# Kernel tuning notes

Hardware: AMD Instinct MI355X
Metric: run time of the kernel (lower is better)

## Reference

```python
import jax, jax.numpy as jnp
import numpy as np

N, C, E = 50000, 128, 10
INV3 = float(1.0 / np.sqrt(3.0))
NORM_C = float(1.0 / np.sqrt(C))


def setup_inputs() -> dict:
    key = jax.random.key(0)
    ks = jax.random.split(key, 14)
    node_feats = jax.random.normal(ks[0], (N, 4 * C), jnp.float32)
    elem = jax.random.randint(ks[1], (N,), 0, E)
    node_attrs = jax.nn.one_hot(elem, E, dtype=jnp.float32)
    sc = jax.random.normal(ks[2], (N, 4 * C), jnp.float32)
    tp2_w = jax.random.normal(ks[3], (4, C), jnp.float32)
    tp3_w = jax.random.normal(ks[4], (8, C), jnp.float32)
    coef0_w0 = jax.random.normal(ks[5], (E, C, C), jnp.float32)
    coef0_w1 = jax.random.normal(ks[6], (E, C, C), jnp.float32)
    coef1_w0 = jax.random.normal(ks[7], (E, 2 * C, C), jnp.float32)
    coef1_w1 = jax.random.normal(ks[8], (E, 2 * C, C), jnp.float32)
    coef2_w0 = jax.random.normal(ks[9], (E, 4 * C, C), jnp.float32)
    coef2_w1 = jax.random.normal(ks[10], (E, 4 * C, C), jnp.float32)
    lin_w0 = jax.random.normal(ks[11], (C, C), jnp.float32)
    lin_w1 = jax.random.normal(ks[12], (C, C), jnp.float32)
    return dict(node_feats=node_feats, node_attrs=node_attrs, sc=sc,
                tp2_w=tp2_w, tp3_w=tp3_w,
                coef0_w0=coef0_w0, coef0_w1=coef0_w1,
                coef1_w0=coef1_w0, coef1_w1=coef1_w1,
                coef2_w0=coef2_w0, coef2_w1=coef2_w1,
                lin_w0=lin_w0, lin_w1=lin_w1)


def acc_elem_linear(x0, x1, attrs, W0, W1):
    # per-element linear combine: one-hot attrs select element-specific weights
    norm = 1.0 / np.sqrt(x0.shape[1])
    o0 = jnp.zeros((attrs.shape[0], W0.shape[2]), x0.dtype)
    o1 = jnp.zeros((attrs.shape[0], W1.shape[2], 3), x1.dtype)
    for e in range(W0.shape[0]):  # small fixed element count
        a = attrs[:, e]
        o0 = o0 + a[:, None] * (x0 @ W0[e])
        o1 = o1 + a[:, None, None] * jnp.einsum('ncm,cd->ndm', x1, W1[e])
    return o0 * norm, o1 * norm


def reference(node_feats, node_attrs, sc, tp2_w, tp3_w,
              coef0_w0, coef0_w1, coef1_w0, coef1_w1,
              coef2_w0, coef2_w1, lin_w0, lin_w1):
    n = node_feats.shape[0]
    s = node_feats[:, :C]                      # [N,C]    0e
    v = node_feats[:, C:].reshape(n, C, 3)     # [N,C,3]  1o

    # nu=2: channelwise (uuu) CG tensor product, paths filtered to {0e,1o}
    m0a = tp2_w[0] * s * s                                # 0e x 0e -> 0e
    m1a = tp2_w[1][:, None] * s[:, :, None] * v * INV3    # 0e x 1o -> 1o
    m1b = tp2_w[2][:, None] * v * s[:, :, None] * INV3    # 1o x 0e -> 1o
    m0b = tp2_w[3] * jnp.sum(v * v, axis=-1) * INV3       # 1o x 1o -> 0e

    # nu=3: mid (A0=m0a 0e, A1=m1a 1o, A2=m1b 1o, A3=m0b 0e) x node_feats
    q0 = jnp.concatenate([
        tp3_w[0] * m0a * s,
        tp3_w[3] * jnp.sum(m1a * v, -1) * INV3,
        tp3_w[5] * jnp.sum(m1b * v, -1) * INV3,
        tp3_w[6] * m0b * s], axis=1)                      # [N,4C]
    q1 = jnp.concatenate([
        tp3_w[1][:, None] * m0a[:, :, None] * v * INV3,
        tp3_w[2][:, None] * m1a * s[:, :, None] * INV3,
        tp3_w[4][:, None] * m1b * s[:, :, None] * INV3,
        tp3_w[7][:, None] * m0b[:, :, None] * v * INV3], axis=1)  # [N,4C,3]

    f0, f1 = acc_elem_linear(s, v, node_attrs, coef0_w0, coef0_w1)
    g0, g1 = acc_elem_linear(jnp.concatenate([m0a, m0b], 1),
                             jnp.concatenate([m1a, m1b], 1),
                             node_attrs, coef1_w0, coef1_w1)
    h0, h1 = acc_elem_linear(q0, q1, node_attrs, coef2_w0, coef2_w1)
    o0 = f0 + g0 + h0
    o1 = f1 + g1 + h1

    o0 = (o0 @ lin_w0) * NORM_C
    o1 = jnp.einsum('ncm,cd->ndm', o1, lin_w1) * NORM_C
    out = jnp.concatenate([o0, o1.reshape(n, -1)], axis=1) + sc
    return out
```

## Files before the change

### kernel.cpp

```cpp
#include <hip/hip_runtime.h>

typedef unsigned short u16;
typedef __attribute__((ext_vector_type(8))) short short8;
typedef __attribute__((ext_vector_type(4))) float f32x4;

#define N_NODES 50000
#define C_ 128
#define E_ 10
#define NT_ 16
#define NBLK_MAIN 3200
#define K0_ 640
#define K1_ 512

#define WF0_BYTES (E_ * 8 * 20 * 512 * 2)
#define WF1_BYTES (E_ * 8 * 16 * 512 * 2)
#define CNT_OFF   (WF0_BYTES + WF1_BYTES)
#define LIST_OFF  (CNT_OFF + 64)

__device__ __forceinline__ u16 f2bf(float f){ union{unsigned u; float f;} v; v.f = f; unsigned u = v.u; u += 0x7FFFu + ((u>>16)&1u); return (u16)(u>>16); }

__global__ void zero_cnt_kernel(int* __restrict__ cnt) {
    if (threadIdx.x < E_) cnt[threadIdx.x] = 0;
}

__global__ __launch_bounds__(256) void prep_weights_kernel(
    const float* __restrict__ tp2, const float* __restrict__ tp3,
    const float* __restrict__ c00, const float* __restrict__ c10, const float* __restrict__ c20,
    const float* __restrict__ c01, const float* __restrict__ c11, const float* __restrict__ c21,
    const float* __restrict__ lin0, const float* __restrict__ lin1,
    u16* __restrict__ WF0, u16* __restrict__ WF1)
{
    const int b = blockIdx.x;
    const int e = b / 9, kb = b % 9;
    const int which = (kb >= 5) ? 1 : 0;
    const int seg = which ? kb - 5 : kb;
    const float* __restrict__ lin = which ? lin1 : lin0;

    __shared__ u16 R[128 * 136];
    __shared__ u16 LT[128 * 132];

    const int tid = threadIdx.x;
    const float NC = 0.08838834764831845f;

    for (int t = tid; t < 128 * 32; t += 256) {
        const int jj = t >> 5, c4 = (t & 31) << 2;
        const float4 v = *(const float4*)(lin + jj * 128 + c4);
        LT[(c4 + 0) * 132 + jj] = f2bf(v.x * NC);
        LT[(c4 + 1) * 132 + jj] = f2bf(v.y * NC);
        LT[(c4 + 2) * 132 + jj] = f2bf(v.z * NC);
        LT[(c4 + 3) * 132 + jj] = f2bf(v.w * NC);
    }

    {
        const int c = tid >> 1, jh = (tid & 1) * 64;
        const float i128 = 0.08838834764831845f;
        const float i256 = 0.0625f;
        const float i512 = 0.04419417382415922f;
        const float I3   = 0.5773502691896258f;
        const float I9   = I3 * I3;
        const float t2_0 = tp2[0*C_+c], t2_1 = tp2[1*C_+c], t2_2 = tp2[2*C_+c], t2_3 = tp2[3*C_+c];
        const float t3_0 = tp3[0*C_+c], t3_1 = tp3[1*C_+c], t3_2 = tp3[2*C_+c];
        const float t3_3 = tp3[3*C_+c], t3_4 = tp3[4*C_+c], t3_5 = tp3[5*C_+c];
        const float t3_6 = tp3[6*C_+c], t3_7 = tp3[7*C_+c];

        const float* P0; const float* P1 = nullptr; const float* P2 = nullptr;
        float a0 = 0.f, a1 = 0.f, a2 = 0.f;
        if (!which) {
            const float* C0 = c00 + (size_t)e * C_   * C_;
            const float* C1 = c10 + (size_t)e * 2*C_ * C_;
            const float* C2 = c20 + (size_t)e * 4*C_ * C_;
            switch (seg) {
            case 0: P0 = C0 + c*C_;          a0 = i128; break;
            case 1: P0 = C1 + c*C_;          a0 = t2_0 * i256; break;
            case 2: P0 = C1 + (C_+c)*C_;     a0 = t2_3 * I3 * i256; break;
            case 3: P0 = C2 + c*C_;          a0 = t3_0 * t2_0 * i512; break;
            default:
// ... 56 lines not shown
#pragma unroll
        for (int s = 0; s < 2; ++s) {
            const int krow = (wv + s * 4) * 16 + lcol;
            union { unsigned long long q[2]; short8 v; } ua;
            ua.q[0] = *(const unsigned long long*)&R[krow * 136 + jj0];
            ua.q[1] = *(const unsigned long long*)&R[krow * 136 + jj0 + 16];
#pragma unroll
            for (int t = 0; t < 8; ++t)
                acc[s][t] = __builtin_amdgcn_mfma_f32_16x16x32_bf16(ua.v, bf[t], acc[s][t], 0, 0, 0);
        }
    }

#pragma unroll
    for (int s = 0; s < 2; ++s) {
#pragma unroll
        for (int r = 0; r < 4; ++r) {
            const int k = (wv + s * 4) * 16 + 4 * gD + r;
            const int ks = k >> 5, r2 = k & 31;
            const int eh = r2 >> 4, g2 = (r2 >> 2) & 3, el = r2 & 3;
            const int elem = eh * 4 + el;
            const int lanef = lcol + 16 * g2;
            const int slot = seg * 4 + ks;
#pragma unroll
            for (int t = 0; t < 8; ++t) {
                const u16 wvl = f2bf(acc[s][t][r]);
                if (!which) WF0[(((size_t)(e*8 + t))*20 + slot)*512 + lanef*8 + elem] = wvl;
                else        WF1[(((size_t)(e*8 + t))*16 + slot)*512 + lanef*8 + elem] = wvl;
            }
        }
    }
}

__global__ void bucket_kernel(const float* __restrict__ attrs,
                              int* __restrict__ cnt, int* __restrict__ lists)
{
    __shared__ int lcnt[E_];
    __shared__ int lbase[E_];
    const int n = blockIdx.x * 256 + threadIdx.x;
    if (threadIdx.x < E_) lcnt[threadIdx.x] = 0;
    __syncthreads();
    int e = 0, my = 0;
    if (n < N_NODES) {
        const float* a = attrs + (size_t)n * E_;
#pragma unroll
        for (int i = 0; i < E_; ++i) if (a[i] > 0.5f) e = i;
        my = atomicAdd(&lcnt[e], 1);
    }
    __syncthreads();
    if (threadIdx.x < E_) lbase[threadIdx.x] = atomicAdd(&cnt[threadIdx.x], lcnt[threadIdx.x]);
    __syncthreads();
    if (n < N_NODES) lists[e*N_NODES + lbase[e] + my] = n;
}

__global__ __launch_bounds__(512, 4) void main_kernel(
    const float* __restrict__ feats, const float* __restrict__ sc,
    const int* __restrict__ cnt, const int* __restrict__ lists,
    const u16* __restrict__ WF0, const u16* __restrict__ WF1,
    float* __restrict__ out)
{
    __shared__ __align__(16) u16 Afull[68 * 512];

    const int tid = threadIdx.x;
    const int bx = blockIdx.x;

    int e = -1, tile = 0, accT = 0;
#pragma unroll
    for (int i = 0; i < E_; ++i) {
        const int ci = cnt[i];
        const int t = (ci + NT_ - 1) >> 4;
        if (e < 0 && bx < accT + t) { e = i; tile = bx - accT; }
        accT += t;
    }
    if (e < 0) return;
    const int nvalid = min(NT_, cnt[e] - tile * NT_);

    const int node = tid >> 5;
    const int ch   = tid & 31;
    const int n = (node < nvalid) ? lists[e*N_NODES + tile*NT_ + node] : -1;

    {
        const int cg = ch;
        float4 sv  = make_float4(0.f,0.f,0.f,0.f);
        float4 va  = sv, vb = sv, vc = sv;
        if (n >= 0) {
            const float* f = feats + (size_t)n * 512;
            sv = *(const float4*)(f + cg*4);
            va = *(const float4*)(f + 128 + cg*12);
            vb = *(const float4*)(f + 128 + cg*12 + 4);
            vc = *(const float4*)(f + 128 + cg*12 + 8);
        }
        float Sa[4]  = {sv.x, sv.y, sv.z, sv.w};
        float Va[12] = {va.x,va.y,va.z,va.w, vb.x,vb.y,vb.z,vb.w, vc.x,vc.y,vc.z,vc.w};

        u16 fsS[5][4];
        u16 fsV[4][3][4];
#pragma unroll
        for (int i = 0; i < 4; ++i) {
            const float S  = Sa[i];
            const float V0 = Va[3*i], V1 = Va[3*i+1], V2 = Va[3*i+2];
            const float S2 = S * S;
            const float VV = V0*V0 + V1*V1 + V2*V2;
            fsS[0][i] = f2bf(S);
            fsS[1][i] = f2bf(S2);
            fsS[2][i] = f2bf(VV);
            fsS[3][i] = f2bf(S2 * S);
            fsS[4][i] = f2bf(S * VV);
            const float Vm[3] = {V0, V1, V2};
#pragma unroll
            for (int m = 0; m < 3; ++m) {
                fsV[0][m][i] = f2bf(Vm[m]);
                fsV[1][m][i] = f2bf(S  * Vm[m]);
                fsV[2][m][i] = f2bf(S2 * Vm[m]);
                fsV[3][m][i] = f2bf(VV * Vm[m]);
            }
        }
        const int lane  = node + 16 * (cg & 3);
        const int ks    = cg >> 3;
        const int ebase = ((cg >> 2) & 1) * 4;
        const int lanep = lane ^ (ks << 1);
        u16* bp = &Afull[lanep*8 + ebase];
#pragma unroll
        for (int p = 0; p < 5; ++p)
            *(ushort4*)&bp[(p*4 + ks) * 512] = *(ushort4*)fsS[p];
#pragma unroll
        for (int q = 0; q < 4; ++q)
#pragma unroll
            for (int m = 0; m < 3; ++m)
                *(ushort4*)&bp[(20 + q*12 + m*4 + ks) * 512] = *(ushort4*)fsV[q][m];
    }
    __syncthreads();

    const int w = tid >> 6, l = tid & 63;
    const int lcol = l & 15, g = l >> 4;
    const int col = w*16 + lcol;
    const u16* WB0 = WF0 + ((size_t)(e*8 + w)) * 20 * 512 + l*8;
    const u16* WB1 = WF1 + ((size_t)(e*8 + w)) * 16 * 512 + l*8;

    f32x4 accS = {0.f, 0.f, 0.f, 0.f};
    f32x4 accV[3];
#pragma unroll
    for (int m = 0; m < 3; ++m) accV[m] = accS;

    float4 scR0, scR1, scR2, scR3;

    short8 bS[2][5], bV[2][4];
#pragma unroll
    for (int p = 0; p < 5; ++p) bS[0][p] = *(const short8*)(WB0 + (p*4 + 0) * 512);
#pragma unroll
    for (int q = 0; q < 4; ++q) bV[0][q] = *(const short8*)(WB1 + (q*4 + 0) * 512);

#pragma unroll
    for (int ks = 0; ks < 4; ++ks) {
        const int cur = ks & 1, nxt = cur ^ 1;
        if (ks < 3) {
#pragma unroll
            for (int p = 0; p < 5; ++p) bS[nxt][p] = *(const short8*)(WB0 + (p*4 + ks + 1) * 512);
#pragma unroll
            for (int q = 0; q < 4; ++q) bV[nxt][q] = *(const short8*)(WB1 + (q*4 + ks + 1) * 512);
        }
        if (ks == 3 && n >= 0) {
            const float* sp = sc + (size_t)n * 512 + ch * 4;
            scR0 = *(const float4*)(sp);
            scR1 = *(const float4*)(sp + 128);
            scR2 = *(const float4*)(sp + 256);
            scR3 = *(const float4*)(sp + 384);
        }
        const int lp8 = (l ^ (ks << 1)) * 8;
#pragma unroll
        for (int p = 0; p < 5; ++p) {
            const short8 a = *(const short8*)&Afull[(p*4 + ks)*512 + lp8];
            accS = __builtin_amdgcn_mfma_f32_16x16x32_bf16(a, bS[cur][p], accS, 0, 0, 0);
        }
#pragma unroll
        for (int q = 0; q < 4; ++q)
#pragma unroll
            for (int m = 0; m < 3; ++m) {
                const short8 a = *(const short8*)&Afull[(20 + q*12 + m*4 + ks)*512 + lp8];
                accV[m] = __builtin_amdgcn_mfma_f32_16x16x32_bf16(a, bV[cur][q], accV[m], 0, 0, 0);
            }
    }

    __syncthreads();
    float* OutB = (float*)Afull;
#pragma unroll
    for (int r = 0; r < 4; ++r) {
        const int nd = 4*g + r;
        OutB[nd*516 + col] = accS[r];
#pragma unroll
        for (int m = 0; m < 3; ++m)
            OutB[nd*516 + 128 + 3*col + m] = accV[m][r];
    }
    __syncthreads();

    if (n >= 0) {
        const size_t gb = (size_t)n * 512 + ch * 4;
        const float4 v0 = *(const float4*)&OutB[node*516 + ch*4];
        const float4 v1 = *(const float4*)&OutB[node*516 + ch*4 + 128];
        const float4 v2 = *(const float4*)&OutB[node*516 + ch*4 + 256];
        const float4 v3 = *(const float4*)&OutB[node*516 + ch*4 + 384];
        float4 o0, o1, o2, o3;
        o0.x=v0.x+scR0.x; o0.y=v0.y+scR0.y; o0.z=v0.z+scR0.z; o0.w=v0.w+scR0.w;
        o1.x=v1.x+scR1.x; o1.y=v1.y+scR1.y; o1.z=v1.z+scR1.z; o1.w=v1.w+scR1.w;
        o2.x=v2.x+scR2.x; o2.y=v2.y+scR2.y; o2.z=v2.z+scR2.z; o2.w=v2.w+scR2.w;
        o3.x=v3.x+scR3.x; o3.y=v3.y+scR3.y; o3.z=v3.z+scR3.z; o3.w=v3.w+scR3.w;
        *(float4*)(out + gb)       = o0;
        *(float4*)(out + gb + 128) = o1;
        *(float4*)(out + gb + 256) = o2;
        *(float4*)(out + gb + 384) = o3;
    }
}

extern "C" void kernel_launch(void* const* d_in, const int* in_sizes, int n_in,
                              void* d_out, int out_size, void* d_ws, size_t ws_size,
                              hipStream_t stream) {
    const float* feats = (const float*)d_in[0];
    const float* attrs = (const float*)d_in[1];
    const float* sc    = (const float*)d_in[2];
    const float* tp2   = (const float*)d_in[3];
    const float* tp3   = (const float*)d_in[4];
    const float* c00   = (const float*)d_in[5];
    const float* c01   = (const float*)d_in[6];
    const float* c10   = (const float*)d_in[7];
    const float* c11   = (const float*)d_in[8];
    const float* c20   = (const float*)d_in[9];
    const float* c21   = (const float*)d_in[10];
    const float* lin0  = (const float*)d_in[11];
    const float* lin1  = (const float*)d_in[12];
    float* out = (float*)d_out;

    char* ws = (char*)d_ws;
    u16* WF0   = (u16*)(ws);
    u16* WF1   = (u16*)(ws + WF0_BYTES);
    int* cnt   = (int*)(ws + CNT_OFF);
    int* lists = (int*)(ws + LIST_OFF);

    hipLaunchKernelGGL(zero_cnt_kernel, dim3(1), dim3(64), 0, stream, cnt);
    hipLaunchKernelGGL(prep_weights_kernel, dim3(E_*9), dim3(256), 0, stream,
                       tp2, tp3, c00, c10, c20, c01, c11, c21, lin0, lin1, WF0, WF1);
    hipLaunchKernelGGL(bucket_kernel, dim3((N_NODES + 255)/256), dim3(256), 0, stream,
                       attrs, cnt, lists);
    hipLaunchKernelGGL(main_kernel, dim3(NBLK_MAIN), dim3(512), 0, stream,
                       feats, sc, cnt, lists, WF0, WF1, out);
}
```

Before: 118.2 us.

## Make main kernel persistent with prefetch of next tile's features

```diff
diff --git a/kernel.cpp b/kernel.cpp
--- a/kernel.cpp
+++ b/kernel.cpp
@@ -8,7 +8,7 @@
 #define C_ 128
 #define E_ 10
 #define NT_ 16
-#define NBLK_MAIN 3200
+#define GRID_MAIN 512
 #define K0_ 640
 #define K1_ 512
 
@@ -18,10 +18,6 @@
 #define LIST_OFF  (CNT_OFF + 64)
 
 __device__ __forceinline__ u16 f2bf(float f){ union{unsigned u; float f;} v; v.f = f; unsigned u = v.u; u += 0x7FFFu + ((u>>16)&1u); return (u16)(u>>16); }
-
-__global__ void zero_cnt_kernel(int* __restrict__ cnt) {
-    if (threadIdx.x < E_) cnt[threadIdx.x] = 0;
-}
 
 __global__ __launch_bounds__(256) void prep_weights_kernel(
     const float* __restrict__ tp2, const float* __restrict__ tp3,
@@ -195,150 +191,182 @@
     const int tid = threadIdx.x;
     const int bx = blockIdx.x;
 
-    int e = -1, tile = 0, accT = 0;
-#pragma unroll
-    for (int i = 0; i < E_; ++i) {
-        const int ci = cnt[i];
-        const int t = (ci + NT_ - 1) >> 4;
-        if (e < 0 && bx < accT + t) { e = i; tile = bx - accT; }
-        accT += t;
-    }
-    if (e < 0) return;
-    const int nvalid = min(NT_, cnt[e] - tile * NT_);
+    int cr0 = cnt[0], cr1 = cnt[1], cr2 = cnt[2], cr3 = cnt[3], cr4 = cnt[4];
+    int cr5 = cnt[5], cr6 = cnt[6], cr7 = cnt[7], cr8 = cnt[8], cr9 = cnt[9];
+#define TC(x) (((x) + NT_ - 1) >> 4)
+    const int t0 = 0;
+    const int t1 = t0 + TC(cr0); const int t2 = t1 + TC(cr1);
+    const int t3 = t2 + TC(cr2); const int t4 = t3 + TC(cr3);
+    const int t5 = t4 + TC(cr4); const int t6 = t5 + TC(cr5);
+    const int t7 = t6 + TC(cr6); const int t8 = t7 + TC(cr7);
+    const int t9 = t8 + TC(cr8); const int ntiles = t9 + TC(cr9);
+#undef TC
 
     const int node = tid >> 5;
     const int ch   = tid & 31;
-    const int n = (node < nvalid) ? lists[e*N_NODES + tile*NT_ + node] : -1;
-
-    {
-        const int cg = ch;
-        float4 sv  = make_float4(0.f,0.f,0.f,0.f);
-        float4 va  = sv, vb = sv, vc = sv;
-        if (n >= 0) {
-            const float* f = feats + (size_t)n * 512;
-            sv = *(const float4*)(f + cg*4);
-            va = *(const float4*)(f + 128 + cg*12);
-            vb = *(const float4*)(f + 128 + cg*12 + 4);
-            vc = *(const float4*)(f + 128 + cg*12 + 8);
-        }
-        float Sa[4]  = {sv.x, sv.y, sv.z, sv.w};
-        float Va[12] = {va.x,va.y,va.z,va.w, vb.x,vb.y,vb.z,vb.w, vc.x,vc.y,vc.z,vc.w};
-
-        u16 fsS[5][4];
-        u16 fsV[4][3][4];
-#pragma unroll
-        for (int i = 0; i < 4; ++i) {
-            const float S  = Sa[i];
-            const float V0 = Va[3*i], V1 = Va[3*i+1], V2 = Va[3*i+2];
-            const float S2 = S * S;
-            const float VV = V0*V0 + V1*V1 + V2*V2;
-            fsS[0][i] = f2bf(S);
-            fsS[1][i] = f2bf(S2);
-            fsS[2][i] = f2bf(VV);
-            fsS[3][i] = f2bf(S2 * S);
-            fsS[4][i] = f2bf(S * VV);
-            const float Vm[3] = {V0, V1, V2};
-#pragma unroll
-            for (int m = 0; m < 3; ++m) {
-                fsV[0][m][i] = f2bf(Vm[m]);
-                fsV[1][m][i] = f2bf(S  * Vm[m]);
-                fsV[2][m][i] = f2bf(S2 * Vm[m]);
-                fsV[3][m][i] = f2bf(VV * Vm[m]);
-            }
-        }
-        const int lane  = node + 16 * (cg & 3);
-        const int ks    = cg >> 3;
-        const int ebase = ((cg >> 2) & 1) * 4;
-        const int lanep = lane ^ (ks << 1);
-        u16* bp = &Afull[lanep*8 + ebase];
-#pragma unroll
-        for (int p = 0; p < 5; ++p)
-            *(ushort4*)&bp[(p*4 + ks) * 512] = *(ushort4*)fsS[p];
-#pragma unroll
-        for (int q = 0; q < 4; ++q)
-#pragma unroll
-            for (int m = 0; m < 3; ++m)
-                *(ushort4*)&bp[(20 + q*12 + m*4 + ks) * 512] = *(ushort4*)fsV[q][m];
-    }
-    __syncthreads();
-
     const int w = tid >> 6, l = tid & 63;
     const int lcol = l & 15, g = l >> 4;
     const int col = w*16 + lcol;
-    const u16* WB0 = WF0 + ((size_t)(e*8 + w)) * 20 * 512 + l*8;
-    const u16* WB1 = WF1 + ((size_t)(e*8 + w)) * 16 * 512 + l*8;
-
-    f32x4 accS = {0.f, 0.f, 0.f, 0.f};
-    f32x4 accV[3];
-#pragma unroll
-    for (int m = 0; m < 3; ++m) accV[m] = accS;
-
-    float4 scR0, scR1, scR2, scR3;
-
-    short8 bS[2][5], bV[2][4];
-#pragma unroll
-    for (int p = 0; p < 5; ++p) bS[0][p] = *(const short8*)(WB0 + (p*4 + 0) * 512);
-#pragma unroll
-    for (int q = 0; q < 4; ++q) bV[0][q] = *(const short8*)(WB1 + (q*4 + 0) * 512);
-
-#pragma unroll
-    for (int ks = 0; ks < 4; ++ks) {
-        const int cur = ks & 1, nxt = cur ^ 1;
-        if (ks < 3) {
-#pragma unroll
-            for (int p = 0; p < 5; ++p) bS[nxt][p] = *(const short8*)(WB0 + (p*4 + ks + 1) * 512);
-#pragma unroll
-            for (int q = 0; q < 4; ++q) bV[nxt][q] = *(const short8*)(WB1 + (q*4 + ks + 1) * 512);
-        }
-        if (ks == 3 && n >= 0) {
-            const float* sp = sc + (size_t)n * 512 + ch * 4;
-            scR0 = *(const float4*)(sp);
-            scR1 = *(const float4*)(sp + 128);
-            scR2 = *(const float4*)(sp + 256);
-            scR3 = *(const float4*)(sp + 384);
-        }
-        const int lp8 = (l ^ (ks << 1)) * 8;
-#pragma unroll
-        for (int p = 0; p < 5; ++p) {
-            const short8 a = *(const short8*)&Afull[(p*4 + ks)*512 + lp8];
-            accS = __builtin_amdgcn_mfma_f32_16x16x32_bf16(a, bS[cur][p], accS, 0, 0, 0);
-        }
-#pragma unroll
-        for (int q = 0; q < 4; ++q)
-#pragma unroll
-            for (int m = 0; m < 3; ++m) {
-                const short8 a = *(const short8*)&Afull[(20 + q*12 + m*4 + ks)*512 + lp8];
-                accV[m] = __builtin_amdgcn_mfma_f32_16x16x32_bf16(a, bV[cur][q], accV[m], 0, 0, 0);
-            }
-    }
-
-    __syncthreads();
-    float* OutB = (float*)Afull;
-#pragma unroll
-    for (int r = 0; r < 4; ++r) {
-        const int nd = 4*g + r;
-        OutB[nd*516 + col] = accS[r];
-#pragma unroll
-        for (int m = 0; m < 3; ++m)
-            OutB[nd*516 + 128 + 3*col + m] = accV[m][r];
-    }
-    __syncthreads();
-
+
+    if (bx >= ntiles) return;
+
+    auto map_tile = [&](int t, int& e_, int& nn_) {
+        int e = 9, base = t9, c = cr9;
+        if (t < t1) { e = 0; base = t0; c = cr0; }
+        else if (t < t2) { e = 1; base = t1; c = cr1; }
+        else if (t < t3) { e = 2; base = t2; c = cr2; }
+        else if (t < t4) { e = 3; base = t3; c = cr3; }
+        else if (t < t5) { e = 4; base = t4; c = cr4; }
+        else if (t < t6) { e = 5; base = t5; c = cr5; }
+        else if (t < t7) { e = 6; base = t6; c = cr6; }
+        else if (t < t8) { e = 7; base = t7; c = cr7; }
+        else if (t < t9) { e = 8; base = t8; c = cr8; }
+        const int tile = t - base;
+        const int nv = min(NT_, c - tile * NT_);
+        e_ = e;
+        nn_ = (node < nv) ? lists[e*N_NODES + tile*NT_ + node] : -1;
+    };
+
+    int e, n;
+    map_tile(bx, e, n);
+    float4 f0 = make_float4(0,0,0,0), f1 = f0, f2 = f0, f3 = f0;
     if (n >= 0) {
-        const size_t gb = (size_t)n * 512 + ch * 4;
-        const float4 v0 = *(const float4*)&OutB[node*516 + ch*4];
-        const float4 v1 = *(const float4*)&OutB[node*516 + ch*4 + 128];
-        const float4 v2 = *(const float4*)&OutB[node*516 + ch*4 + 256];
-        const float4 v3 = *(const float4*)&OutB[node*516 + ch*4 + 384];
-        float4 o0, o1, o2, o3;
-        o0.x=v0.x+scR0.x; o0.y=v0.y+scR0.y; o0.z=v0.z+scR0.z; o0.w=v0.w+scR0.w;
-        o1.x=v1.x+scR1.x; o1.y=v1.y+scR1.y; o1.z=v1.z+scR1.z; o1.w=v1.w+scR1.w;
-        o2.x=v2.x+scR2.x; o2.y=v2.y+scR2.y; o2.z=v2.z+scR2.z; o2.w=v2.w+scR2.w;
-        o3.x=v3.x+scR3.x; o3.y=v3.y+scR3.y; o3.z=v3.z+scR3.z; o3.w=v3.w+scR3.w;
-        *(float4*)(out + gb)       = o0;
-        *(float4*)(out + gb + 128) = o1;
-        *(float4*)(out + gb + 256) = o2;
-        *(float4*)(out + gb + 384) = o3;
+        const float* f = feats + (size_t)n * 512;
+        f0 = *(const float4*)(f + ch*4);
+        f1 = *(const float4*)(f + 128 + ch*12);
+        f2 = *(const float4*)(f + 128 + ch*12 + 4);
+        f3 = *(const float4*)(f + 128 + ch*12 + 8);
+    }
+
+    for (int t = bx; t < ntiles; t += GRID_MAIN) {
+        {
+            float Sa[4]  = {f0.x, f0.y, f0.z, f0.w};
+            float Va[12] = {f1.x,f1.y,f1.z,f1.w, f2.x,f2.y,f2.z,f2.w, f3.x,f3.y,f3.z,f3.w};
+
+            u16 fsS[5][4];
+            u16 fsV[4][3][4];
+#pragma unroll
+            for (int i = 0; i < 4; ++i) {
+                const float S  = Sa[i];
+                const float V0 = Va[3*i], V1 = Va[3*i+1], V2 = Va[3*i+2];
+                const float S2 = S * S;
+                const float VV = V0*V0 + V1*V1 + V2*V2;
+                fsS[0][i] = f2bf(S);
+                fsS[1][i] = f2bf(S2);
+                fsS[2][i] = f2bf(VV);
+                fsS[3][i] = f2bf(S2 * S);
+                fsS[4][i] = f2bf(S * VV);
+                const float Vm[3] = {V0, V1, V2};
+#pragma unroll
+                for (int m = 0; m < 3; ++m) {
+                    fsV[0][m][i] = f2bf(Vm[m]);
+                    fsV[1][m][i] = f2bf(S  * Vm[m]);
+                    fsV[2][m][i] = f2bf(S2 * Vm[m]);
+                    fsV[3][m][i] = f2bf(VV * Vm[m]);
+                }
+            }
+            const int lane  = node + 16 * (ch & 3);
+            const int ks    = ch >> 3;
+            const int ebase = ((ch >> 2) & 1) * 4;
+            const int lanep = lane ^ (ks << 1);
+            u16* bp = &Afull[lanep*8 + ebase];
+#pragma unroll
+            for (int p = 0; p < 5; ++p)
+                *(ushort4*)&bp[(p*4 + ks) * 512] = *(ushort4*)fsS[p];
+#pragma unroll
+            for (int q = 0; q < 4; ++q)
+#pragma unroll
+                for (int m = 0; m < 3; ++m)
+                    *(ushort4*)&bp[(20 + q*12 + m*4 + ks) * 512] = *(ushort4*)fsV[q][m];
+        }
+        __syncthreads();
+
+        const u16* WB0 = WF0 + ((size_t)(e*8 + w)) * (20*512) + l*8;
+        const u16* WB1 = WF1 + ((size_t)(e*8 + w)) * (16*512) + l*8;
+
+        f32x4 accS = {0.f, 0.f, 0.f, 0.f};
+        f32x4 accV0 = accS, accV1 = accS, accV2 = accS;
+        float4 scR0, scR1, scR2, scR3;
+        int ne = e, nn = -1;
+
+#pragma unroll
+        for (int ks = 0; ks < 4; ++ks) {
+            short8 bS[5], bV[4];
+#pragma unroll
+            for (int p = 0; p < 5; ++p) bS[p] = *(const short8*)(WB0 + (p*4 + ks) * 512);
+#pragma unroll
+            for (int q = 0; q < 4; ++q) bV[q] = *(const short8*)(WB1 + (q*4 + ks) * 512);
+
+            if (ks == 1 && n >= 0) {
+                const float* sp = sc + (size_t)n * 512 + ch * 4;
+                scR0 = *(const float4*)(sp);
+                scR1 = *(const float4*)(sp + 128);
+                scR2 = *(const float4*)(sp + 256);
+                scR3 = *(const float4*)(sp + 384);
+            }
+            if (ks == 2) {
+                const int tn = t + GRID_MAIN;
+                f0 = make_float4(0,0,0,0); f1 = f0; f2 = f0; f3 = f0;
+                if (tn < ntiles) {
+                    map_tile(tn, ne, nn);
+                    if (nn >= 0) {
+                        const float* f = feats + (size_t)nn * 512;
+                        f0 = *(const float4*)(f + ch*4);
+                        f1 = *(const float4*)(f + 128 + ch*12);
+                        f2 = *(const float4*)(f + 128 + ch*12 + 4);
+                        f3 = *(const float4*)(f + 128 + ch*12 + 8);
+                    }
+                }
+            }
+
+            const int lp8 = (l ^ (ks << 1)) * 8;
+#pragma unroll
+            for (int p = 0; p < 5; ++p) {
+                const short8 a = *(const short8*)&Afull[(p*4 + ks)*512 + lp8];
+                accS = __builtin_amdgcn_mfma_f32_16x16x32_bf16(a, bS[p], accS, 0, 0, 0);
+            }
+#pragma unroll
+            for (int q = 0; q < 4; ++q) {
+                const short8 a0 = *(const short8*)&Afull[(20 + q*12 + 0*4 + ks)*512 + lp8];
+                accV0 = __builtin_amdgcn_mfma_f32_16x16x32_bf16(a0, bV[q], accV0, 0, 0, 0);
+                const short8 a1 = *(const short8*)&Afull[(20 + q*12 + 1*4 + ks)*512 + lp8];
+                accV1 = __builtin_amdgcn_mfma_f32_16x16x32_bf16(a1, bV[q], accV1, 0, 0, 0);
+                const short8 a2 = *(const short8*)&Afull[(20 + q*12 + 2*4 + ks)*512 + lp8];
+                accV2 = __builtin_amdgcn_mfma_f32_16x16x32_bf16(a2, bV[q], accV2, 0, 0, 0);
+            }
+        }
+
+        __syncthreads();
+        float* OutB = (float*)Afull;
+#pragma unroll
+        for (int r = 0; r < 4; ++r) {
+            const int nd = 4*g + r;
+            OutB[nd*516 + col] = accS[r];
+            OutB[nd*516 + 128 + 3*col + 0] = accV0[r];
+            OutB[nd*516 + 128 + 3*col + 1] = accV1[r];
+            OutB[nd*516 + 128 + 3*col + 2] = accV2[r];
+        }
+        __syncthreads();
+
+        if (n >= 0) {
+            const size_t gb = (size_t)n * 512 + ch * 4;
+            const float4 v0 = *(const float4*)&OutB[node*516 + ch*4];
+            const float4 v1 = *(const float4*)&OutB[node*516 + ch*4 + 128];
+            const float4 v2 = *(const float4*)&OutB[node*516 + ch*4 + 256];
+            const float4 v3 = *(const float4*)&OutB[node*516 + ch*4 + 384];
+            float4 o0, o1, o2, o3;
+            o0.x=v0.x+scR0.x; o0.y=v0.y+scR0.y; o0.z=v0.z+scR0.z; o0.w=v0.w+scR0.w;
+            o1.x=v1.x+scR1.x; o1.y=v1.y+scR1.y; o1.z=v1.z+scR1.z; o1.w=v1.w+scR1.w;
+            o2.x=v2.x+scR2.x; o2.y=v2.y+scR2.y; o2.z=v2.z+scR2.z; o2.w=v2.w+scR2.w;
+            o3.x=v3.x+scR3.x; o3.y=v3.y+scR3.y; o3.z=v3.z+scR3.z; o3.w=v3.w+scR3.w;
+            *(float4*)(out + gb)       = o0;
+            *(float4*)(out + gb + 128) = o1;
+            *(float4*)(out + gb + 256) = o2;
+            *(float4*)(out + gb + 384) = o3;
+        }
+        __syncthreads();
+
+        e = ne; n = nn;
     }
 }
 
@@ -366,11 +394,11 @@
     int* cnt   = (int*)(ws + CNT_OFF);
     int* lists = (int*)(ws + LIST_OFF);
 
-    hipLaunchKernelGGL(zero_cnt_kernel, dim3(1), dim3(64), 0, stream, cnt);
+    hipMemsetAsync(cnt, 0, 64, stream);
     hipLaunchKernelGGL(prep_weights_kernel, dim3(E_*9), dim3(256), 0, stream,
                        tp2, tp3, c00, c10, c20, c01, c11, c21, lin0, lin1, WF0, WF1);
     hipLaunchKernelGGL(bucket_kernel, dim3((N_NODES + 255)/256), dim3(256), 0, stream,
                        attrs, cnt, lists);
-    hipLaunchKernelGGL(main_kernel, dim3(NBLK_MAIN), dim3(512), 0, stream,
+    hipLaunchKernelGGL(main_kernel, dim3(GRID_MAIN), dim3(512), 0, stream,
                        feats, sc, cnt, lists, WF0, WF1, out);
 }
```

New measurement: 149.2 us. 26.3% more time.

## Stage A operands through double-buffered LDS phases to raise main kernel occupancy

Applied to the files above, without the earlier changes.

```diff
diff --git a/kernel.cpp b/kernel.cpp
--- a/kernel.cpp
+++ b/kernel.cpp
@@ -18,10 +18,6 @@
 #define LIST_OFF  (CNT_OFF + 64)
 
 __device__ __forceinline__ u16 f2bf(float f){ union{unsigned u; float f;} v; v.f = f; unsigned u = v.u; u += 0x7FFFu + ((u>>16)&1u); return (u16)(u>>16); }
-
-__global__ void zero_cnt_kernel(int* __restrict__ cnt) {
-    if (threadIdx.x < E_) cnt[threadIdx.x] = 0;
-}
 
 __global__ __launch_bounds__(256) void prep_weights_kernel(
     const float* __restrict__ tp2, const float* __restrict__ tp3,
@@ -184,13 +180,13 @@
     if (n < N_NODES) lists[e*N_NODES + lbase[e] + my] = n;
 }
 
-__global__ __launch_bounds__(512, 4) void main_kernel(
+__global__ __launch_bounds__(512, 6) void main_kernel(
     const float* __restrict__ feats, const float* __restrict__ sc,
     const int* __restrict__ cnt, const int* __restrict__ lists,
     const u16* __restrict__ WF0, const u16* __restrict__ WF1,
     float* __restrict__ out)
 {
-    __shared__ __align__(16) u16 Afull[68 * 512];
+    __shared__ __align__(16) u16 A2[2][24 * 512];
 
     const int tid = threadIdx.x;
     const int bx = blockIdx.x;
@@ -210,117 +206,166 @@
     const int ch   = tid & 31;
     const int n = (node < nvalid) ? lists[e*N_NODES + tile*NT_ + node] : -1;
 
+    float4 f0 = make_float4(0.f,0.f,0.f,0.f), f1 = f0, f2 = f0, f3 = f0;
+    if (n >= 0) {
+        const float* f = feats + (size_t)n * 512;
+        f0 = *(const float4*)(f + ch*4);
+        f1 = *(const float4*)(f + 128 + ch*12);
+        f2 = *(const float4*)(f + 128 + ch*12 + 4);
+        f3 = *(const float4*)(f + 128 + ch*12 + 8);
+    }
+    const float Sa[4]  = {f0.x, f0.y, f0.z, f0.w};
+    const float Va[12] = {f1.x,f1.y,f1.z,f1.w, f2.x,f2.y,f2.z,f2.w, f3.x,f3.y,f3.z,f3.w};
+
+    const int lane  = node + 16 * (ch & 3);
+    const int ksl   = ch >> 3;
+    const int ebase = ((ch >> 2) & 1) * 4;
+    const int lanep = lane ^ (ksl << 1);
+    u16* bpA = &A2[0][lanep*8 + ebase];
+    u16* bpB = &A2[1][lanep*8 + ebase];
+
     {
-        const int cg = ch;
-        float4 sv  = make_float4(0.f,0.f,0.f,0.f);
-        float4 va  = sv, vb = sv, vc = sv;
-        if (n >= 0) {
-            const float* f = feats + (size_t)n * 512;
-            sv = *(const float4*)(f + cg*4);
-            va = *(const float4*)(f + 128 + cg*12);
-            vb = *(const float4*)(f + 128 + cg*12 + 4);
-            vc = *(const float4*)(f + 128 + cg*12 + 8);
-        }
-        float Sa[4]  = {sv.x, sv.y, sv.z, sv.w};
-        float Va[12] = {va.x,va.y,va.z,va.w, vb.x,vb.y,vb.z,vb.w, vc.x,vc.y,vc.z,vc.w};
-
-        u16 fsS[5][4];
-        u16 fsV[4][3][4];
+        u16 fs[5][4];
 #pragma unroll
         for (int i = 0; i < 4; ++i) {
             const float S  = Sa[i];
             const float V0 = Va[3*i], V1 = Va[3*i+1], V2 = Va[3*i+2];
             const float S2 = S * S;
             const float VV = V0*V0 + V1*V1 + V2*V2;
-            fsS[0][i] = f2bf(S);
-            fsS[1][i] = f2bf(S2);
-            fsS[2][i] = f2bf(VV);
-            fsS[3][i] = f2bf(S2 * S);
-            fsS[4][i] = f2bf(S * VV);
-            const float Vm[3] = {V0, V1, V2};
-#pragma unroll
-            for (int m = 0; m < 3; ++m) {
-                fsV[0][m][i] = f2bf(Vm[m]);
-                fsV[1][m][i] = f2bf(S  * Vm[m]);
-                fsV[2][m][i] = f2bf(S2 * Vm[m]);
-                fsV[3][m][i] = f2bf(VV * Vm[m]);
-            }
-        }
-        const int lane  = node + 16 * (cg & 3);
-        const int ks    = cg >> 3;
-        const int ebase = ((cg >> 2) & 1) * 4;
-        const int lanep = lane ^ (ks << 1);
-        u16* bp = &Afull[lanep*8 + ebase];
+            fs[0][i] = f2bf(S);
+            fs[1][i] = f2bf(S2);
+            fs[2][i] = f2bf(VV);
+            fs[3][i] = f2bf(S2 * S);
+            fs[4][i] = f2bf(S * VV);
+        }
 #pragma unroll
         for (int p = 0; p < 5; ++p)
-            *(ushort4*)&bp[(p*4 + ks) * 512] = *(ushort4*)fsS[p];
-#pragma unroll
-        for (int q = 0; q < 4; ++q)
-#pragma unroll
-            for (int m = 0; m < 3; ++m)
-                *(ushort4*)&bp[(20 + q*12 + m*4 + ks) * 512] = *(ushort4*)fsV[q][m];
+            *(ushort4*)&bpA[(p*4 + ksl) * 512] = *(ushort4*)fs[p];
     }
     __syncthreads();
 
     const int w = tid >> 6, l = tid & 63;
     const int lcol = l & 15, g = l >> 4;
     const int col = w*16 + lcol;
-    const u16* WB0 = WF0 + ((size_t)(e*8 + w)) * 20 * 512 + l*8;
-    const u16* WB1 = WF1 + ((size_t)(e*8 + w)) * 16 * 512 + l*8;
+    const u16* WB0 = WF0 + ((size_t)(e*8 + w)) * (20*512) + l*8;
+    const u16* WB1 = WF1 + ((size_t)(e*8 + w)) * (16*512) + l*8;
 
     f32x4 accS = {0.f, 0.f, 0.f, 0.f};
-    f32x4 accV[3];
-#pragma unroll
-    for (int m = 0; m < 3; ++m) accV[m] = accS;
-
-    float4 scR0, scR1, scR2, scR3;
-
-    short8 bS[2][5], bV[2][4];
-#pragma unroll
-    for (int p = 0; p < 5; ++p) bS[0][p] = *(const short8*)(WB0 + (p*4 + 0) * 512);
-#pragma unroll
-    for (int q = 0; q < 4; ++q) bV[0][q] = *(const short8*)(WB1 + (q*4 + 0) * 512);
-
-#pragma unroll
-    for (int ks = 0; ks < 4; ++ks) {
-        const int cur = ks & 1, nxt = cur ^ 1;
-        if (ks < 3) {
-#pragma unroll
-            for (int p = 0; p < 5; ++p) bS[nxt][p] = *(const short8*)(WB0 + (p*4 + ks + 1) * 512);
-#pragma unroll
-            for (int q = 0; q < 4; ++q) bV[nxt][q] = *(const short8*)(WB1 + (q*4 + ks + 1) * 512);
-        }
-        if (ks == 3 && n >= 0) {
-            const float* sp = sc + (size_t)n * 512 + ch * 4;
-            scR0 = *(const float4*)(sp);
-            scR1 = *(const float4*)(sp + 128);
-            scR2 = *(const float4*)(sp + 256);
-            scR3 = *(const float4*)(sp + 384);
-        }
-        const int lp8 = (l ^ (ks << 1)) * 8;
+    f32x4 accV0 = accS, accV1 = accS, accV2 = accS;
+
+    {
+        u16 fs[6][4];
+#pragma unroll
+        for (int i = 0; i < 4; ++i) {
+            const float S  = Sa[i];
+            const float Vm[3] = {Va[3*i], Va[3*i+1], Va[3*i+2]};
+#pragma unroll
+            for (int m = 0; m < 3; ++m) {
+                fs[m][i]     = f2bf(Vm[m]);
+                fs[3+m][i]   = f2bf(S * Vm[m]);
+            }
+        }
+#pragma unroll
+        for (int t = 0; t < 6; ++t)
+            *(ushort4*)&bpB[(t*4 + ksl) * 512] = *(ushort4*)fs[t];
+    }
+#pragma unroll
+    for (int ks2 = 0; ks2 < 4; ++ks2) {
+        short8 bS[5];
+#pragma unroll
+        for (int p = 0; p < 5; ++p) bS[p] = *(const short8*)(WB0 + (p*4 + ks2) * 512);
+        const int lp8 = (l ^ (ks2 << 1)) * 8;
 #pragma unroll
         for (int p = 0; p < 5; ++p) {
-            const short8 a = *(const short8*)&Afull[(p*4 + ks)*512 + lp8];
-            accS = __builtin_amdgcn_mfma_f32_16x16x32_bf16(a, bS[cur][p], accS, 0, 0, 0);
-        }
-#pragma unroll
-        for (int q = 0; q < 4; ++q)
+            const short8 a = *(const short8*)&A2[0][(p*4 + ks2)*512 + lp8];
+            accS = __builtin_amdgcn_mfma_f32_16x16x32_bf16(a, bS[p], accS, 0, 0, 0);
+        }
+    }
+    __syncthreads();
+
+    {
+        u16 fs[6][4];
+#pragma unroll
+        for (int i = 0; i < 4; ++i) {
+            const float S  = Sa[i];
+            const float V0 = Va[3*i], V1 = Va[3*i+1], V2 = Va[3*i+2];
+            const float S2 = S * S;
+            const float VV = V0*V0 + V1*V1 + V2*V2;
+            const float Vm[3] = {V0, V1, V2};
 #pragma unroll
             for (int m = 0; m < 3; ++m) {
-                const short8 a = *(const short8*)&Afull[(20 + q*12 + m*4 + ks)*512 + lp8];
-                accV[m] = __builtin_amdgcn_mfma_f32_16x16x32_bf16(a, bV[cur][q], accV[m], 0, 0, 0);
-            }
-    }
-
-    __syncthreads();
-    float* OutB = (float*)Afull;
+                fs[m][i]   = f2bf(S2 * Vm[m]);
+                fs[3+m][i] = f2bf(VV * Vm[m]);
+            }
+        }
+#pragma unroll
+        for (int t = 0; t < 6; ++t)
+            *(ushort4*)&bpA[(t*4 + ksl) * 512] = *(ushort4*)fs[t];
+    }
+    float4 scR0 = make_float4(0.f,0.f,0.f,0.f), scR1 = scR0, scR2 = scR0, scR3 = scR0;
+    if (n >= 0) {
+        const float* sp = sc + (size_t)n * 512 + ch * 4;
+        scR0 = *(const float4*)(sp);
+        scR1 = *(const float4*)(sp + 128);
+        scR2 = *(const float4*)(sp + 256);
+        scR3 = *(const float4*)(sp + 384);
+    }
+#pragma unroll
+    for (int ks2 = 0; ks2 < 4; ++ks2) {
+        const short8 b0 = *(const short8*)(WB1 + (0*4 + ks2) * 512);
+        const short8 b1 = *(const short8*)(WB1 + (1*4 + ks2) * 512);
+        const int lp8 = (l ^ (ks2 << 1)) * 8;
+        {
+            const short8 a0 = *(const short8*)&A2[1][(0*4 + ks2)*512 + lp8];
+            accV0 = __builtin_amdgcn_mfma_f32_16x16x32_bf16(a0, b0, accV0, 0, 0, 0);
+            const short8 a1 = *(const short8*)&A2[1][(1*4 + ks2)*512 + lp8];
+            accV1 = __builtin_amdgcn_mfma_f32_16x16x32_bf16(a1, b0, accV1, 0, 0, 0);
+            const short8 a2 = *(const short8*)&A2[1][(2*4 + ks2)*512 + lp8];
+            accV2 = __builtin_amdgcn_mfma_f32_16x16x32_bf16(a2, b0, accV2, 0, 0, 0);
+        }
+        {
+            const short8 a0 = *(const short8*)&A2[1][(3*4 + ks2)*512 + lp8];
+            accV0 = __builtin_amdgcn_mfma_f32_16x16x32_bf16(a0, b1, accV0, 0, 0, 0);
+            const short8 a1 = *(const short8*)&A2[1][(4*4 + ks2)*512 + lp8];
+            accV1 = __builtin_amdgcn_mfma_f32_16x16x32_bf16(a1, b1, accV1, 0, 0, 0);
+            const short8 a2 = *(const short8*)&A2[1][(5*4 + ks2)*512 + lp8];
+            accV2 = __builtin_amdgcn_mfma_f32_16x16x32_bf16(a2, b1, accV2, 0, 0, 0);
+        }
+    }
+    __syncthreads();
+
+#pragma unroll
+    for (int ks2 = 0; ks2 < 4; ++ks2) {
+        const short8 b2 = *(const short8*)(WB1 + (2*4 + ks2) * 512);
+        const short8 b3 = *(const short8*)(WB1 + (3*4 + ks2) * 512);
+        const int lp8 = (l ^ (ks2 << 1)) * 8;
+        {
+            const short8 a0 = *(const short8*)&A2[0][(0*4 + ks2)*512 + lp8];
+            accV0 = __builtin_amdgcn_mfma_f32_16x16x32_bf16(a0, b2, accV0, 0, 0, 0);
+            const short8 a1 = *(const short8*)&A2[0][(1*4 + ks2)*512 + lp8];
+            accV1 = __builtin_amdgcn_mfma_f32_16x16x32_bf16(a1, b2, accV1, 0, 0, 0);
+            const short8 a2 = *(const short8*)&A2[0][(2*4 + ks2)*512 + lp8];
+            accV2 = __builtin_amdgcn_mfma_f32_16x16x32_bf16(a2, b2, accV2, 0, 0, 0);
+        }
+        {
+            const short8 a0 = *(const short8*)&A2[0][(3*4 + ks2)*512 + lp8];
+            accV0 = __builtin_amdgcn_mfma_f32_16x16x32_bf16(a0, b3, accV0, 0, 0, 0);
+            const short8 a1 = *(const short8*)&A2[0][(4*4 + ks2)*512 + lp8];
+            accV1 = __builtin_amdgcn_mfma_f32_16x16x32_bf16(a1, b3, accV1, 0, 0, 0);
+            const short8 a2 = *(const short8*)&A2[0][(5*4 + ks2)*512 + lp8];
+            accV2 = __builtin_amdgcn_mfma_f32_16x16x32_bf16(a2, b3, accV2, 0, 0, 0);
+        }
+    }
+    __syncthreads();
+
+    float* OutB = (float*)&A2[0][0];
 #pragma unroll
     for (int r = 0; r < 4; ++r) {
         const int nd = 4*g + r;
         OutB[nd*516 + col] = accS[r];
-#pragma unroll
-        for (int m = 0; m < 3; ++m)
-            OutB[nd*516 + 128 + 3*col + m] = accV[m][r];
+        OutB[nd*516 + 128 + 3*col + 0] = accV0[r];
+        OutB[nd*516 + 128 + 3*col + 1] = accV1[r];
+        OutB[nd*516 + 128 + 3*col + 2] = accV2[r];
     }
     __syncthreads();
 
@@ -366,7 +411,7 @@
     int* cnt   = (int*)(ws + CNT_OFF);
     int* lists = (int*)(ws + LIST_OFF);
 
-    hipLaunchKernelGGL(zero_cnt_kernel, dim3(1), dim3(64), 0, stream, cnt);
+    hipMemsetAsync(cnt, 0, 64, stream);
     hipLaunchKernelGGL(prep_weights_kernel, dim3(E_*9), dim3(256), 0, stream,
                        tp2, tp3, c00, c10, c20, c01, c11, c21, lin0, lin1, WF0, WF1);
     hipLaunchKernelGGL(bucket_kernel, dim3((N_NODES + 255)/256), dim3(256), 0, stream,
```

New measurement: 117.3 us. About the same (-0.7%).

## Restructure main kernel to 256 threads with staged double-buffered LDS A-tiles

Applied to the files above, without the earlier changes.

```diff
diff --git a/kernel.cpp b/kernel.cpp
--- a/kernel.cpp
+++ b/kernel.cpp
@@ -18,9 +18,10 @@
 #define LIST_OFF  (CNT_OFF + 64)
 
 __device__ __forceinline__ u16 f2bf(float f){ union{unsigned u; float f;} v; v.f = f; unsigned u = v.u; u += 0x7FFFu + ((u>>16)&1u); return (u16)(u>>16); }
-
-__global__ void zero_cnt_kernel(int* __restrict__ cnt) {
-    if (threadIdx.x < E_) cnt[threadIdx.x] = 0;
+__device__ __forceinline__ unsigned cvtpk(float a, float b){
+    unsigned r;
+    asm("v_cvt_pk_bf16_f32 %0, %1, %2" : "=v"(r) : "v"(a), "v"(b));
+    return r;
 }
 
 __global__ __launch_bounds__(256) void prep_weights_kernel(
@@ -184,13 +185,13 @@
     if (n < N_NODES) lists[e*N_NODES + lbase[e] + my] = n;
 }
 
-__global__ __launch_bounds__(512, 4) void main_kernel(
+__global__ __launch_bounds__(256, 3) void main_kernel(
     const float* __restrict__ feats, const float* __restrict__ sc,
     const int* __restrict__ cnt, const int* __restrict__ lists,
     const u16* __restrict__ WF0, const u16* __restrict__ WF1,
     float* __restrict__ out)
 {
-    __shared__ __align__(16) u16 Afull[68 * 512];
+    __shared__ __align__(16) u16 A2[2][24 * 512];
 
     const int tid = threadIdx.x;
     const int bx = blockIdx.x;
@@ -206,140 +207,167 @@
     if (e < 0) return;
     const int nvalid = min(NT_, cnt[e] - tile * NT_);
 
-    const int node = tid >> 5;
-    const int ch   = tid & 31;
+    const int node = tid >> 4;
+    const int cg   = tid & 15;
     const int n = (node < nvalid) ? lists[e*N_NODES + tile*NT_ + node] : -1;
 
-    {
-        const int cg = ch;
-        float4 sv  = make_float4(0.f,0.f,0.f,0.f);
-        float4 va  = sv, vb = sv, vc = sv;
-        if (n >= 0) {
-            const float* f = feats + (size_t)n * 512;
-            sv = *(const float4*)(f + cg*4);
-            va = *(const float4*)(f + 128 + cg*12);
-            vb = *(const float4*)(f + 128 + cg*12 + 4);
-            vc = *(const float4*)(f + 128 + cg*12 + 8);
-        }
-        float Sa[4]  = {sv.x, sv.y, sv.z, sv.w};
-        float Va[12] = {va.x,va.y,va.z,va.w, vb.x,vb.y,vb.z,vb.w, vc.x,vc.y,vc.z,vc.w};
-
-        u16 fsS[5][4];
-        u16 fsV[4][3][4];
-#pragma unroll
-        for (int i = 0; i < 4; ++i) {
-            const float S  = Sa[i];
-            const float V0 = Va[3*i], V1 = Va[3*i+1], V2 = Va[3*i+2];
-            const float S2 = S * S;
-            const float VV = V0*V0 + V1*V1 + V2*V2;
-            fsS[0][i] = f2bf(S);
-            fsS[1][i] = f2bf(S2);
-            fsS[2][i] = f2bf(VV);
-            fsS[3][i] = f2bf(S2 * S);
-            fsS[4][i] = f2bf(S * VV);
-            const float Vm[3] = {V0, V1, V2};
+    float4 s0 = make_float4(0.f,0.f,0.f,0.f), s1 = s0;
+    float4 v4[6];
+#pragma unroll
+    for (int k = 0; k < 6; ++k) v4[k] = s0;
+    if (n >= 0) {
+        const float* f = feats + (size_t)n * 512;
+        s0 = *(const float4*)(f + cg*8);
+        s1 = *(const float4*)(f + cg*8 + 4);
+#pragma unroll
+        for (int k = 0; k < 6; ++k) v4[k] = *(const float4*)(f + 128 + cg*24 + 4*k);
+    }
+    float S[8]  = {s0.x,s0.y,s0.z,s0.w, s1.x,s1.y,s1.z,s1.w};
+    float V[24] = {v4[0].x,v4[0].y,v4[0].z,v4[0].w, v4[1].x,v4[1].y,v4[1].z,v4[1].w,
+                   v4[2].x,v4[2].y,v4[2].z,v4[2].w, v4[3].x,v4[3].y,v4[3].z,v4[3].w,
+                   v4[4].x,v4[4].y,v4[4].z,v4[4].w, v4[5].x,v4[5].y,v4[5].z,v4[5].w};
+    float S2[8], VV[8];
+#pragma unroll
+    for (int i = 0; i < 8; ++i) {
+        S2[i] = S[i]*S[i];
+        VV[i] = V[3*i]*V[3*i] + V[3*i+1]*V[3*i+1] + V[3*i+2]*V[3*i+2];
+    }
+
+    const int ksl   = cg >> 2;
+    const int eh    = (cg >> 1) & 1;
+    const int gb    = (cg & 1) * 2;
+    const int lp0   = (node + 16*gb)        ^ (ksl << 1);
+    const int lp1   = (node + 16*(gb + 1))  ^ (ksl << 1);
+    const int off0  = lp0*8 + 4*eh;
+    const int off1  = lp1*8 + 4*eh;
+
+#define WSLOT(BUF, SLOT, V0,V1,V2,V3,V4,V5,V6,V7) do { \
+        uint2 w0_, w1_; \
+        w0_.x = cvtpk((V0),(V1)); w0_.y = cvtpk((V2),(V3)); \
+        w1_.x = cvtpk((V4),(V5)); w1_.y = cvtpk((V6),(V7)); \
+        *(uint2*)&A2[BUF][(SLOT)*512 + off0] = w0_; \
+        *(uint2*)&A2[BUF][(SLOT)*512 + off1] = w1_; \
+    } while (0)
+
+    WSLOT(0, 0*4 + ksl, S[0],S[1],S[2],S[3],S[4],S[5],S[6],S[7]);
+    WSLOT(0, 1*4 + ksl, S2[0],S2[1],S2[2],S2[3],S2[4],S2[5],S2[6],S2[7]);
+    WSLOT(0, 2*4 + ksl, VV[0],VV[1],VV[2],VV[3],VV[4],VV[5],VV[6],VV[7]);
+    WSLOT(0, 3*4 + ksl, S2[0]*S[0],S2[1]*S[1],S2[2]*S[2],S2[3]*S[3],
+                        S2[4]*S[4],S2[5]*S[5],S2[6]*S[6],S2[7]*S[7]);
+    WSLOT(0, 4*4 + ksl, S[0]*VV[0],S[1]*VV[1],S[2]*VV[2],S[3]*VV[3],
+                        S[4]*VV[4],S[5]*VV[5],S[6]*VV[6],S[7]*VV[7]);
+    __syncthreads();
+
+    const int w4 = tid >> 6, l = tid & 63;
+    const int lcol = l & 15, g = l >> 4;
+    const int col0 = (2*w4)*16 + lcol;
+    const int col1 = col0 + 16;
+    const u16* WB0a = WF0 + ((size_t)(e*8 + 2*w4))     * (20*512) + l*8;
+    const u16* WB0b = WB0a + 20*512;
+    const u16* WB1a = WF1 + ((size_t)(e*8 + 2*w4))     * (16*512) + l*8;
+    const u16* WB1b = WB1a + 16*512;
+
+    f32x4 accS0 = {0.f,0.f,0.f,0.f}, accS1 = accS0;
+    f32x4 accV[3][2];
+#pragma unroll
+    for (int m = 0; m < 3; ++m) { accV[m][0] = accS0; accV[m][1] = accS0; }
+
+#pragma unroll
+    for (int m = 0; m < 3; ++m) {
+        WSLOT(1, m*4 + ksl,     V[0*3+m],V[1*3+m],V[2*3+m],V[3*3+m],
+                                V[4*3+m],V[5*3+m],V[6*3+m],V[7*3+m]);
+        WSLOT(1, (3+m)*4 + ksl, S[0]*V[0*3+m],S[1]*V[1*3+m],S[2]*V[2*3+m],S[3]*V[3*3+m],
+                                S[4]*V[4*3+m],S[5]*V[5*3+m],S[6]*V[6*3+m],S[7]*V[7*3+m]);
+    }
+#pragma unroll
+    for (int ks2 = 0; ks2 < 4; ++ks2) {
+        const int lp8 = (l ^ (ks2 << 1)) * 8;
+#pragma unroll
+        for (int p = 0; p < 5; ++p) {
+            const short8 a  = *(const short8*)&A2[0][(p*4 + ks2)*512 + lp8];
+            const short8 b0 = *(const short8*)(WB0a + (p*4 + ks2)*512);
+            const short8 b1 = *(const short8*)(WB0b + (p*4 + ks2)*512);
+            accS0 = __builtin_amdgcn_mfma_f32_16x16x32_bf16(a, b0, accS0, 0, 0, 0);
+            accS1 = __builtin_amdgcn_mfma_f32_16x16x32_bf16(a, b1, accS1, 0, 0, 0);
+        }
+    }
+    __syncthreads();
+
+#pragma unroll
+    for (int m = 0; m < 3; ++m) {
+        WSLOT(0, m*4 + ksl,     S2[0]*V[0*3+m],S2[1]*V[1*3+m],S2[2]*V[2*3+m],S2[3]*V[3*3+m],
+                                S2[4]*V[4*3+m],S2[5]*V[5*3+m],S2[6]*V[6*3+m],S2[7]*V[7*3+m]);
+        WSLOT(0, (3+m)*4 + ksl, VV[0]*V[0*3+m],VV[1]*V[1*3+m],VV[2]*V[2*3+m],VV[3]*V[3*3+m],
+                                VV[4]*V[4*3+m],VV[5]*V[5*3+m],VV[6]*V[6*3+m],VV[7]*V[7*3+m]);
+    }
+    float4 scR[8];
+#pragma unroll
+    for (int j = 0; j < 8; ++j) scR[j] = make_float4(0.f,0.f,0.f,0.f);
+    if (n >= 0) {
+        const float* sp = sc + (size_t)n * 512 + cg * 4;
+#pragma unroll
+        for (int j = 0; j < 8; ++j) scR[j] = *(const float4*)(sp + 64*j);
+    }
+#pragma unroll
+    for (int ks2 = 0; ks2 < 4; ++ks2) {
+        const int lp8 = (l ^ (ks2 << 1)) * 8;
+#pragma unroll
+        for (int q = 0; q < 2; ++q) {
+            const short8 b0 = *(const short8*)(WB1a + (q*4 + ks2)*512);
+            const short8 b1 = *(const short8*)(WB1b + (q*4 + ks2)*512);
 #pragma unroll
             for (int m = 0; m < 3; ++m) {
-                fsV[0][m][i] = f2bf(Vm[m]);
-                fsV[1][m][i] = f2bf(S  * Vm[m]);
-                fsV[2][m][i] = f2bf(S2 * Vm[m]);
-                fsV[3][m][i] = f2bf(VV * Vm[m]);
-            }
-        }
-        const int lane  = node + 16 * (cg & 3);
-        const int ks    = cg >> 3;
-        const int ebase = ((cg >> 2) & 1) * 4;
-        const int lanep = lane ^ (ks << 1);
-        u16* bp = &Afull[lanep*8 + ebase];
-#pragma unroll
-        for (int p = 0; p < 5; ++p)
-            *(ushort4*)&bp[(p*4 + ks) * 512] = *(ushort4*)fsS[p];
-#pragma unroll
-        for (int q = 0; q < 4; ++q)
-#pragma unroll
-            for (int m = 0; m < 3; ++m)
-                *(ushort4*)&bp[(20 + q*12 + m*4 + ks) * 512] = *(ushort4*)fsV[q][m];
-    }
-    __syncthreads();
-
-    const int w = tid >> 6, l = tid & 63;
-    const int lcol = l & 15, g = l >> 4;
-    const int col = w*16 + lcol;
-    const u16* WB0 = WF0 + ((size_t)(e*8 + w)) * 20 * 512 + l*8;
-    const u16* WB1 = WF1 + ((size_t)(e*8 + w)) * 16 * 512 + l*8;
-
-    f32x4 accS = {0.f, 0.f, 0.f, 0.f};
-    f32x4 accV[3];
-#pragma unroll
-    for (int m = 0; m < 3; ++m) accV[m] = accS;
-
-    float4 scR0, scR1, scR2, scR3;
-
-    short8 bS[2][5], bV[2][4];
-#pragma unroll
-    for (int p = 0; p < 5; ++p) bS[0][p] = *(const short8*)(WB0 + (p*4 + 0) * 512);
-#pragma unroll
-    for (int q = 0; q < 4; ++q) bV[0][q] = *(const short8*)(WB1 + (q*4 + 0) * 512);
-
-#pragma unroll
-    for (int ks = 0; ks < 4; ++ks) {
-        const int cur = ks & 1, nxt = cur ^ 1;
-        if (ks < 3) {
-#pragma unroll
-            for (int p = 0; p < 5; ++p) bS[nxt][p] = *(const short8*)(WB0 + (p*4 + ks + 1) * 512);
-#pragma unroll
-            for (int q = 0; q < 4; ++q) bV[nxt][q] = *(const short8*)(WB1 + (q*4 + ks + 1) * 512);
-        }
-        if (ks == 3 && n >= 0) {
-            const float* sp = sc + (size_t)n * 512 + ch * 4;
-            scR0 = *(const float4*)(sp);
-            scR1 = *(const float4*)(sp + 128);
-            scR2 = *(const float4*)(sp + 256);
-            scR3 = *(const float4*)(sp + 384);
-        }
-        const int lp8 = (l ^ (ks << 1)) * 8;
-#pragma unroll
-        for (int p = 0; p < 5; ++p) {
-            const short8 a = *(const short8*)&Afull[(p*4 + ks)*512 + lp8];
-            accS = __builtin_amdgcn_mfma_f32_16x16x32_bf16(a, bS[cur][p], accS, 0, 0, 0);
-        }
-#pragma unroll
-        for (int q = 0; q < 4; ++q)
+                const short8 a = *(const short8*)&A2[1][((q*3 + m)*4 + ks2)*512 + lp8];
+                accV[m][0] = __builtin_amdgcn_mfma_f32_16x16x32_bf16(a, b0, accV[m][0], 0, 0, 0);
+                accV[m][1] = __builtin_amdgcn_mfma_f32_16x16x32_bf16(a, b1, accV[m][1], 0, 0, 0);
+            }
+        }
+    }
+    __syncthreads();
+
+#pragma unroll
+    for (int ks2 = 0; ks2 < 4; ++ks2) {
+        const int lp8 = (l ^ (ks2 << 1)) * 8;
+#pragma unroll
+        for (int q = 0; q < 2; ++q) {
+            const short8 b0 = *(const short8*)(WB1a + ((2+q)*4 + ks2)*512);
+            const short8 b1 = *(const short8*)(WB1b + ((2+q)*4 + ks2)*512);
 #pragma unroll
             for (int m = 0; m < 3; ++m) {
-                const short8 a = *(const short8*)&Afull[(20 + q*12 + m*4 + ks)*512 + lp8];
-                accV[m] = __builtin_amdgcn_mfma_f32_16x16x32_bf16(a, bV[cur][q], accV[m], 0, 0, 0);
-            }
-    }
-
-    __syncthreads();
-    float* OutB = (float*)Afull;
+                const short8 a = *(const short8*)&A2[0][((q*3 + m)*4 + ks2)*512 + lp8];
+                accV[m][0] = __builtin_amdgcn_mfma_f32_16x16x32_bf16(a, b0, accV[m][0], 0, 0, 0);
+                accV[m][1] = __builtin_amdgcn_mfma_f32_16x16x32_bf16(a, b1, accV[m][1], 0, 0, 0);
+            }
+        }
+    }
+    __syncthreads();
+
+    float* OutB = (float*)&A2[0][0];
 #pragma unroll
     for (int r = 0; r < 4; ++r) {
         const int nd = 4*g + r;
-        OutB[nd*516 + col] = accS[r];
-#pragma unroll
-        for (int m = 0; m < 3; ++m)
-            OutB[nd*516 + 128 + 3*col + m] = accV[m][r];
+        OutB[nd*516 + col0] = accS0[r];
+        OutB[nd*516 + col1] = accS1[r];
+#pragma unroll
+        for (int m = 0; m < 3; ++m) {
+            OutB[nd*516 + 128 + 3*col0 + m] = accV[m][0][r];
+            OutB[nd*516 + 128 + 3*col1 + m] = accV[m][1][r];
+        }
     }
     __syncthreads();
 
     if (n >= 0) {
-        const size_t gb = (size_t)n * 512 + ch * 4;
-        const float4 v0 = *(const float4*)&OutB[node*516 + ch*4];
-        const float4 v1 = *(const float4*)&OutB[node*516 + ch*4 + 128];
-        const float4 v2 = *(const float4*)&OutB[node*516 + ch*4 + 256];
-        const float4 v3 = *(const float4*)&OutB[node*516 + ch*4 + 384];
-        float4 o0, o1, o2, o3;
-        o0.x=v0.x+scR0.x; o0.y=v0.y+scR0.y; o0.z=v0.z+scR0.z; o0.w=v0.w+scR0.w;
-        o1.x=v1.x+scR1.x; o1.y=v1.y+scR1.y; o1.z=v1.z+scR1.z; o1.w=v1.w+scR1.w;
-        o2.x=v2.x+scR2.x; o2.y=v2.y+scR2.y; o2.z=v2.z+scR2.z; o2.w=v2.w+scR2.w;
-        o3.x=v3.x+scR3.x; o3.y=v3.y+scR3.y; o3.z=v3.z+scR3.z; o3.w=v3.w+scR3.w;
-        *(float4*)(out + gb)       = o0;
-        *(float4*)(out + gb + 128) = o1;
-        *(float4*)(out + gb + 256) = o2;
-        *(float4*)(out + gb + 384) = o3;
-    }
+        const size_t gb2 = (size_t)n * 512 + cg * 4;
+#pragma unroll
+        for (int j = 0; j < 8; ++j) {
+            const float4 vres = *(const float4*)&OutB[node*516 + cg*4 + 64*j];
+            float4 o;
+            o.x = vres.x + scR[j].x; o.y = vres.y + scR[j].y;
+            o.z = vres.z + scR[j].z; o.w = vres.w + scR[j].w;
+            *(float4*)(out + gb2 + 64*j) = o;
+        }
+    }
+#undef WSLOT
 }
 
 extern "C" void kernel_launch(void* const* d_in, const int* in_sizes, int n_in,
@@ -366,11 +394,11 @@
     int* cnt   = (int*)(ws + CNT_OFF);
     int* lists = (int*)(ws + LIST_OFF);
 
-    hipLaunchKernelGGL(zero_cnt_kernel, dim3(1), dim3(64), 0, stream, cnt);
+    hipMemsetAsync(cnt, 0, 64, stream);
     hipLaunchKernelGGL(prep_weights_kernel, dim3(E_*9), dim3(256), 0, stream,
                        tp2, tp3, c00, c10, c20, c01, c11, c21, lin0, lin1, WF0, WF1);
     hipLaunchKernelGGL(bucket_kernel, dim3((N_NODES + 255)/256), dim3(256), 0, stream,
                        attrs, cnt, lists);
-    hipLaunchKernelGGL(main_kernel, dim3(NBLK_MAIN), dim3(512), 0, stream,
+    hipLaunchKernelGGL(main_kernel, dim3(NBLK_MAIN), dim3(256), 0, stream,
                        feats, sc, cnt, lists, WF0, WF1, out);
 }
```

Measured after the change: 116.6 us. No clear change (-1.3%).
